# Optimization experiments

Measured on AMD Instinct MI355X. Metric: run time of the kernel, lower is better.

## Reference

```python
import jax, jax.numpy as jnp
import numpy as np
from jax import lax

N_HEAD = 8
C_CLIP = 10.0
NEG_INF = -jnp.inf


def setup_inputs() -> dict:
    key = jax.random.key(0)
    ks = jax.random.split(key, 12)
    B, S, E = 1024, 200, 128
    bound = 1.0 / E
    inp = {
        "encoded_inputs": jax.random.normal(ks[0], (B, S, E), dtype=jnp.float32),
        "demands": jax.random.uniform(ks[1], (B, S), dtype=jnp.float32),
        "capacities": jax.random.uniform(ks[2], (B,), dtype=jnp.float32),
        # learned params
        "vl": jax.random.uniform(ks[3], (1, 1, E), minval=-bound, maxval=bound, dtype=jnp.float32),
        "vf": jax.random.uniform(ks[4], (1, 1, E), minval=-bound, maxval=bound, dtype=jnp.float32),
        "Wq": jax.random.normal(ks[5], (3 * E, E), dtype=jnp.float32) / np.sqrt(3 * E),
        "Wk": jax.random.normal(ks[6], (E, E), dtype=jnp.float32) / np.sqrt(E),
        "Wv": jax.random.normal(ks[7], (E, E), dtype=jnp.float32) / np.sqrt(E),
        "Wo": jax.random.normal(ks[8], (E, E), dtype=jnp.float32) / np.sqrt(E),
        "Wp": jax.random.normal(ks[9], (E, E), dtype=jnp.float32) / np.sqrt(E),  # project_k (no bias)
    }
    return inp


def _decode(encoded_inputs, vl, vf, Wq, Wk, Wv, Wo, Wp):
    B, S, E = encoded_inputs.shape
    H = N_HEAD
    dh = E // H
    scale = jnp.sqrt(jnp.float32(E))
    h_hat = encoded_inputs.mean(axis=1)                       # [B,E] (context mean)
    # keys/values for glimpse MHA and pointer keys are loop-invariant
    k_h = (encoded_inputs @ Wk).reshape(B, S, H, dh).transpose(0, 2, 1, 3)  # [B,H,S,dh]
    v_h = (encoded_inputs @ Wv).reshape(B, S, H, dh).transpose(0, 2, 1, 3)  # [B,H,S,dh]
    k_ptr = encoded_inputs @ Wp                               # [B,S,E]

    mask0 = jnp.zeros((B, S), dtype=bool).at[:, 0].set(True)
    last0 = jnp.broadcast_to(vl[0, 0], (B, E))
    first0 = jnp.broadcast_to(vf[0, 0], (B, E))
    logp0 = jnp.zeros((B,), dtype=jnp.float32)
    rows = jnp.arange(B)

    def step(carry, t):
        mask, last, first, logp = carry
        h_c = jnp.concatenate([h_hat, last, first], axis=-1)  # [B,3E]
        q = (h_c @ Wq).reshape(B, H, dh)
        scores = jnp.einsum('bhd,bhsd->bhs', q, k_h) / jnp.sqrt(jnp.float32(dh))
        scores = jnp.where(mask[:, None, :], NEG_INF, scores)
        attn = jax.nn.softmax(scores, axis=-1)
        ctx = jnp.einsum('bhs,bhsd->bhd', attn, v_h).reshape(B, E) @ Wo   # [B,E]
        u = jnp.tanh(jnp.einsum('be,bse->bs', ctx, k_ptr) / scale) * C_CLIP  # [B,S] raw logits
        u_masked = jnp.where(mask, NEG_INF, u)
        idx = jnp.argmax(u_masked, axis=-1)                   # greedy decoding
        ce = -jnp.take_along_axis(jax.nn.log_softmax(u_masked, axis=-1), idx[:, None], axis=1)[:, 0]
        logp = logp + ce
        last_new = encoded_inputs[rows, idx]                  # [B,E]
        mask_new = mask.at[rows, idx].set(True)
        first_new = jnp.where(t == 0, last_new, first)
        return (mask_new, last_new, first_new, logp), (u, idx)

    (_, _, _, log_probabilities), (raw_u, sols) = lax.scan(
        step, (mask0, last0, first0, logp0), jnp.arange(S - 1))
    raw_logits = raw_u.transpose(1, 0, 2)                     # [B, S-1, S]
    solution = jnp.concatenate([jnp.zeros((B, 1), jnp.int32), sols.T.astype(jnp.int32)], axis=1)
    return raw_logits, log_probabilities, solution


def reference(encoded_inputs, demands, capacities, vl, vf, Wq, Wk, Wv, Wo, Wp):
    # demands/capacities are part of the input tuple but unused by this forward
    return _decode(encoded_inputs, vl, vf, Wq, Wk, Wv, Wo, Wp)
```

## Files before the change

kernel.cpp:

```cpp
#include <hip/hip_runtime.h>
#include <cmath>

constexpr int Bn = 1024, Sn = 200, En = 128, Hn = 8, DHn = 16, Tn = 199;
constexpr long long LOGITS_N = (long long)Bn * Tn * Sn;
constexpr long long LOGP_OFF = LOGITS_N;
constexpr long long SOL_OFF  = LOGP_OFF + Bn;

#define NEG_INF (-__builtin_inff())

__device__ __forceinline__ float dot4(float4 a, float4 b) {
  return a.x * b.x + a.y * b.y + a.z * b.z + a.w * b.w;
}

__global__ __launch_bounds__(128) void hhat_kernel(
    const float* __restrict__ enc, const float* __restrict__ vl, const float* __restrict__ vf,
    const float* __restrict__ Wq, float* __restrict__ qtop, float* __restrict__ qh0)
{
  const int b = blockIdx.x, e = threadIdx.x;
  const float* p = enc + (size_t)b * Sn * En + e;
  float s = 0.f;
  for (int i = 0; i < Sn; ++i) s += p[(size_t)i * En];
  __shared__ float hl[En];
  hl[e] = s * (1.0f / Sn);
  __syncthreads();
  float qt = 0.f, qm = 0.f, qf = 0.f;
#pragma unroll 8
  for (int i = 0; i < En; ++i) {
    qt += hl[i] * Wq[i * En + e];
    qm += vl[i] * Wq[(En + i) * En + e];
    qf += vf[i] * Wq[(2 * En + i) * En + e];
  }
  qtop[(size_t)b * En + e] = qt;
  qh0[(size_t)b * En + e]  = qt + qm + qf;
}

__global__ __launch_bounds__(256) void proj_kernel(
    const float* __restrict__ enc,
    const float* __restrict__ Wk, const float* __restrict__ Wv,
    const float* __restrict__ Wq, const float* __restrict__ Wp,
    float* __restrict__ Kall, float* __restrict__ Vall,
    float* __restrict__ QM, float* __restrict__ KP2)
{
  __shared__ float et[32 * En];
  __shared__ float wl[En * En];
  const int tid = threadIdx.x;
  const size_t r0 = (size_t)blockIdx.x * 32;

  for (int i = tid; i < 32 * En; i += 256) et[i] = enc[r0 * En + i];

  const float* Ws[4] = {Wk, Wv, Wq + (size_t)En * En, Wp};
  float* Os[3] = {Kall, Vall, QM};
  for (int m = 0; m < 4; ++m) {
    __syncthreads();
    const float* W = Ws[m];
    for (int i = tid; i < En * En; i += 256) wl[i] = W[i];
    __syncthreads();
    const int j = tid & 127, half = tid >> 7;
    for (int rr = 0; rr < 16; ++rr) {
      const int r = rr * 2 + half;
      float a0 = 0.f, a1 = 0.f, a2 = 0.f, a3 = 0.f;
#pragma unroll 8
      for (int e = 0; e < En; e += 4) {
        a0 += et[r * En + e    ] * wl[(e    ) * En + j];
        a1 += et[r * En + e + 1] * wl[(e + 1) * En + j];
        a2 += et[r * En + e + 2] * wl[(e + 2) * En + j];
        a3 += et[r * En + e + 3] * wl[(e + 3) * En + j];
      }
      const float a = (a0 + a1) + (a2 + a3);
      const size_t rg = r0 + r;
      if (m < 3) {
        Os[m][rg * En + j] = a;
      } else {
        const int b = (int)(rg / Sn), s = (int)(rg - (size_t)b * Sn);
        KP2[(((size_t)b * 32 + (j >> 2)) * Sn + s) * 4 + (j & 3)] = a;
      }
    }
  }
}

__global__ __launch_bounds__(512, 2) void decode_kernel(
    const float* __restrict__ enc, const float* __restrict__ Wq, const float* __restrict__ Wo,
    const float* __restrict__ Kall, const float* __restrict__ Vall,
    const float* __restrict__ KP2, const float* __restrict__ QM,
    const float* __restrict__ qtop, const float* __restrict__ qh0,
    float* __restrict__ out)
{
  const int b = blockIdx.x, tid = threadIdx.x;
  const int w = tid >> 6, lane = tid & 63;
  const int le = lane & 15, q4 = lane >> 4;

  __shared__ __align__(16) float kp2[32 * Sn * 4];
  __shared__ __align__(16) float qv[En];
  __shared__ __align__(16) float octx[En];
  __shared__ float hqf[En];
  __shared__ float ctxs[En];
  __shared__ float uvals[256];
  __shared__ int   smask[256];
  __shared__ int   idx_s;
  __shared__ float logp_s;

  {
    const float4* src = (const float4*)(KP2 + (size_t)b * (32 * Sn * 4));
    float4* dst = (float4*)kp2;
    for (int i = tid; i < 32 * Sn; i += 512) dst[i] = src[i];
  }
  float Kr[4][16], Vr[4][16];
#pragma unroll
  for (int j = 0; j < 4; ++j) {
    const int s = j * 64 + lane;
    if (s < Sn) {
      const float4* kq = (const float4*)(Kall + ((size_t)b * Sn + s) * En + w * DHn);
      const float4* vq = (const float4*)(Vall + ((size_t)b * Sn + s) * En + w * DHn);
#pragma unroll
      for (int q = 0; q < 4; ++q) {
        const float4 kv = kq[q], vv = vq[q];
        Kr[j][4*q+0] = kv.x; Kr[j][4*q+1] = kv.y; Kr[j][4*q+2] = kv.z; Kr[j][4*q+3] = kv.w;
        Vr[j][4*q+0] = vv.x; Vr[j][4*q+1] = vv.y; Vr[j][4*q+2] = vv.z; Vr[j][4*q+3] = vv.w;
      }
    } else {
#pragma unroll
      for (int d = 0; d < 16; ++d) { Kr[j][d] = 0.f; Vr[j][d] = 0.f; }
    }
  }
  float WoR[32];
  {
    const float* wp = Wo + (size_t)(q4 * 32) * En + (w * DHn + le);
#pragma unroll
    for (int r = 0; r < 32; ++r) WoR[r] = wp[(size_t)r * En];
  }
  if (tid < 256) smask[tid] = (tid == 0) ? 1 : 0;
  if (tid < En)  qv[tid] = qh0[(size_t)b * En + tid];
  if (tid == 0) { logp_s = 0.f; out[SOL_OFF + (size_t)b * Sn] = 0.f; }
  __syncthreads();

  for (int t = 0; t < Tn; ++t) {
    float qs[16];
    {
      const float4* qp = (const float4*)&qv[w * DHn];
#pragma unroll
      for (int q = 0; q < 4; ++q) {
        const float4 v = qp[q];
        qs[4*q+0] = v.x; qs[4*q+1] = v.y; qs[4*q+2] = v.z; qs[4*q+3] = v.w;
      }
    }
    float sc[4];
#pragma unroll
    for (int j = 0; j < 4; ++j) {
      const int s = j * 64 + lane;
      float a = 0.f;
#pragma unroll
      for (int d = 0; d < 16; ++d) a += qs[d] * Kr[j][d];
      sc[j] = (s >= Sn || smask[s]) ? NEG_INF : a * 0.25f;
    }
    float m = fmaxf(fmaxf(sc[0], sc[1]), fmaxf(sc[2], sc[3]));
#pragma unroll
    for (int off = 1; off < 64; off <<= 1) m = fmaxf(m, __shfl_xor(m, off));
    float ev[4]; float sum = 0.f;
#pragma unroll
    for (int j = 0; j < 4; ++j) { ev[j] = expf(sc[j] - m); sum += ev[j]; }
#pragma unroll
    for (int off = 1; off < 64; off <<= 1) sum += __shfl_xor(sum, off);
    const float inv = 1.f / sum;

    float acc[16];
#pragma unroll
    for (int d = 0; d < 16; ++d) acc[d] = 0.f;
#pragma unroll
    for (int j = 0; j < 4; ++j) {
      const float aj = ev[j] * inv;
#pragma unroll
      for (int d = 0; d < 16; ++d) acc[d] += aj * Vr[j][d];
    }
#pragma unroll
    for (int off = 1; off < 64; off <<= 1) {
#pragma unroll
      for (int d = 0; d < 16; ++d) acc[d] += __shfl_xor(acc[d], off);
    }
    if (lane == 0) {
#pragma unroll
      for (int d = 0; d < 16; ++d) ctxs[w * DHn + d] = acc[d];
    }
    __syncthreads();

    {
      float p = 0.f;
      const float* cb = &ctxs[q4 * 32];
#pragma unroll
      for (int r = 0; r < 32; ++r) p += cb[r] * WoR[r];
      p += __shfl_xor(p, 16);
      p += __shfl_xor(p, 32);
      if (lane < 16) octx[w * DHn + le] = p;
    }
    __syncthreads();

    {
      const int sp = tid >> 1, hf = tid & 1;
      float p = 0.f;
      if (sp < Sn) {
        const float4* oc = (const float4*)&octx[hf * 64];
#pragma unroll
        for (int e4 = 0; e4 < 16; ++e4)
          p += dot4(oc[e4], *(const float4*)&kp2[(((hf * 16 + e4) * Sn) + sp) << 2]);
      }
      p += __shfl_xor(p, 1);
      if (!hf) {
        if (sp < Sn) {
          const float uu = tanhf(p * 0.08838834764831845f) * 10.f;
          out[((size_t)b * Tn + t) * Sn + sp] = uu;
          uvals[sp] = smask[sp] ? NEG_INF : uu;
        } else uvals[sp] = NEG_INF;
      }
    }
    __syncthreads();

    if (w == 0) {
      float bv = NEG_INF; int bi = 1 << 30;
#pragma unroll
      for (int k = 0; k < 4; ++k) {
        const int s = lane + 64 * k;
        const float v = uvals[s];
        if (v > bv || (v == bv && s < bi)) { bv = v; bi = s; }
      }
#pragma unroll
      for (int off = 1; off < 64; off <<= 1) {
        const float ovv = __shfl_xor(bv, off); const int oi = __shfl_xor(bi, off);
        if (ovv > bv || (ovv == bv && oi < bi)) { bv = ovv; bi = oi; }
      }
      float sum2 = 0.f;
#pragma unroll
      for (int k = 0; k < 4; ++k) sum2 += expf(uvals[lane + 64 * k] - bv);
#pragma unroll
      for (int off = 1; off < 64; off <<= 1) sum2 += __shfl_xor(sum2, off);
      if (lane == 0) {
        idx_s = bi;
        logp_s += logf(sum2);
        out[SOL_OFF + (size_t)b * Sn + t + 1] = (float)bi;
      }
    }
    __syncthreads();

    const int idx = idx_s;
    if (tid == 0) smask[idx] = 1;

    if (t == 0) {
      if (tid < En) uvals[tid] = enc[((size_t)b * Sn + idx) * En + tid];
      __syncthreads();
      {
        float p = 0.f;
        const float* er  = &uvals[q4 * 32];
        const float* wqb = Wq + (size_t)(2 * En + q4 * 32) * En + (w * DHn + le);
#pragma unroll
        for (int r = 0; r < 32; ++r) p += er[r] * wqb[(size_t)r * En];
        p += __shfl_xor(p, 16);
        p += __shfl_xor(p, 32);
        if (lane < 16) hqf[w * DHn + le] = qtop[(size_t)b * En + (w * DHn + le)] + p;
      }
      __syncthreads();
    }

    if (t + 1 < Tn) {
      if (tid < En) qv[tid] = hqf[tid] + QM[((size_t)b * Sn + idx) * En + tid];
    }
    __syncthreads();
  }
  if (tid == 0) out[LOGP_OFF + b] = logp_s;
}

extern "C" void kernel_launch(void* const* d_in, const int* in_sizes, int n_in,
                              void* d_out, int out_size, void* d_ws, size_t ws_size,
                              hipStream_t stream)
{
  const float* enc = (const float*)d_in[0];
  const float* vl  = (const float*)d_in[3];
  const float* vf  = (const float*)d_in[4];
  const float* Wq  = (const float*)d_in[5];
  const float* Wk  = (const float*)d_in[6];
  const float* Wv  = (const float*)d_in[7];
  const float* Wo  = (const float*)d_in[8];
  const float* Wp  = (const float*)d_in[9];
  float* out = (float*)d_out;

  float* ws   = (float*)d_ws;
  const size_t BSE = (size_t)Bn * Sn * En;
  float* Kall = ws;
  float* Vall = Kall + BSE;
  float* QM   = Vall + BSE;
  float* KP2  = QM   + BSE;
  float* qtop = KP2  + BSE;
  float* qh0  = qtop + (size_t)Bn * En;

  hipLaunchKernelGGL(hhat_kernel, dim3(Bn), dim3(En), 0, stream, enc, vl, vf, Wq, qtop, qh0);
  hipLaunchKernelGGL(proj_kernel, dim3((Bn * Sn) / 32), dim3(256), 0, stream,
                     enc, Wk, Wv, Wq, Wp, Kall, Vall, QM, KP2);
  hipLaunchKernelGGL(decode_kernel, dim3(Bn), dim3(512), 0, stream,
                     enc, Wq, Wo, Kall, Vall, KP2, QM, qtop, qh0, out);
}
```

Baseline: 6.255 ms.

## Restructure decode loop: register-resident pointer keys, shared QM, fewer barriers

The decode kernel now keeps the pointer-key projection in registers, split per head-wave, instead of in shared memory. It stages the QM table in LDS so the next-step query is formed in place. The mask moves into per-lane register bits, argmax runs redundantly in every wave to drop a barrier, the ctx reduction uses a transpose-style butterfly, and tanh/exp switch to fast intrinsics. The projection kernel is re-tiled to register-block 16 rows and to write K/V in the head-interleaved layout. The cost is higher register pressure (three 64-float arrays per thread), a launch-bounds change that drops the 2-blocks hint, and about 100KB of LDS per block.

```diff
diff --git a/kernel.cpp b/kernel.cpp
--- a/kernel.cpp
+++ b/kernel.cpp
@@ -7,10 +7,6 @@
 constexpr long long SOL_OFF  = LOGP_OFF + Bn;
 
 #define NEG_INF (-__builtin_inff())
-
-__device__ __forceinline__ float dot4(float4 a, float4 b) {
-  return a.x * b.x + a.y * b.y + a.z * b.z + a.w * b.w;
-}
 
 __global__ __launch_bounds__(128) void hhat_kernel(
     const float* __restrict__ enc, const float* __restrict__ vl, const float* __restrict__ vf,
@@ -38,7 +34,7 @@
     const float* __restrict__ enc,
     const float* __restrict__ Wk, const float* __restrict__ Wv,
     const float* __restrict__ Wq, const float* __restrict__ Wp,
-    float* __restrict__ Kall, float* __restrict__ Vall,
+    float* __restrict__ K2, float* __restrict__ V2,
     float* __restrict__ QM, float* __restrict__ KP2)
 {
   __shared__ float et[32 * En];
@@ -49,38 +45,43 @@
   for (int i = tid; i < 32 * En; i += 256) et[i] = enc[r0 * En + i];
 
   const float* Ws[4] = {Wk, Wv, Wq + (size_t)En * En, Wp};
-  float* Os[3] = {Kall, Vall, QM};
+  const int j = tid & 127, half = tid >> 7;
   for (int m = 0; m < 4; ++m) {
     __syncthreads();
     const float* W = Ws[m];
     for (int i = tid; i < En * En; i += 256) wl[i] = W[i];
     __syncthreads();
-    const int j = tid & 127, half = tid >> 7;
-    for (int rr = 0; rr < 16; ++rr) {
-      const int r = rr * 2 + half;
-      float a0 = 0.f, a1 = 0.f, a2 = 0.f, a3 = 0.f;
-#pragma unroll 8
-      for (int e = 0; e < En; e += 4) {
-        a0 += et[r * En + e    ] * wl[(e    ) * En + j];
-        a1 += et[r * En + e + 1] * wl[(e + 1) * En + j];
-        a2 += et[r * En + e + 2] * wl[(e + 2) * En + j];
-        a3 += et[r * En + e + 3] * wl[(e + 3) * En + j];
-      }
-      const float a = (a0 + a1) + (a2 + a3);
-      const size_t rg = r0 + r;
-      if (m < 3) {
-        Os[m][rg * En + j] = a;
+    float a[16];
+#pragma unroll
+    for (int r = 0; r < 16; ++r) a[r] = 0.f;
+    for (int e = 0; e < En; e += 4) {
+      const float w0 = wl[(e    ) * En + j];
+      const float w1 = wl[(e + 1) * En + j];
+      const float w2 = wl[(e + 2) * En + j];
+      const float w3 = wl[(e + 3) * En + j];
+#pragma unroll
+      for (int r = 0; r < 16; ++r) {
+        const float4 e4 = *(const float4*)&et[(r * 2 + half) * En + e];
+        a[r] += e4.x * w0 + e4.y * w1 + e4.z * w2 + e4.w * w3;
+      }
+    }
+#pragma unroll
+    for (int r = 0; r < 16; ++r) {
+      const size_t rg = r0 + r * 2 + half;
+      const int b = (int)(rg / Sn), s = (int)(rg - (size_t)b * Sn);
+      if (m == 2) {
+        QM[rg * En + j] = a[r];
       } else {
-        const int b = (int)(rg / Sn), s = (int)(rg - (size_t)b * Sn);
-        KP2[(((size_t)b * 32 + (j >> 2)) * Sn + s) * 4 + (j & 3)] = a;
+        float* o = (m == 0) ? K2 : (m == 1) ? V2 : KP2;
+        o[(((size_t)b * 32 + (j >> 2)) * Sn + s) * 4 + (j & 3)] = a[r];
       }
     }
   }
 }
 
-__global__ __launch_bounds__(512, 2) void decode_kernel(
+__global__ __launch_bounds__(512) void decode_kernel(
     const float* __restrict__ enc, const float* __restrict__ Wq, const float* __restrict__ Wo,
-    const float* __restrict__ Kall, const float* __restrict__ Vall,
+    const float* __restrict__ K2, const float* __restrict__ V2,
     const float* __restrict__ KP2, const float* __restrict__ QM,
     const float* __restrict__ qtop, const float* __restrict__ qh0,
     float* __restrict__ out)
@@ -88,38 +89,42 @@
   const int b = blockIdx.x, tid = threadIdx.x;
   const int w = tid >> 6, lane = tid & 63;
   const int le = lane & 15, q4 = lane >> 4;
-
-  __shared__ __align__(16) float kp2[32 * Sn * 4];
-  __shared__ __align__(16) float qv[En];
-  __shared__ __align__(16) float octx[En];
+  const int dm = ((le & 1) << 3) | ((le & 2) << 1) | ((le & 4) >> 1) | ((le & 8) >> 3);
+
+  __shared__ __align__(16) float qmL[Sn * En];
+  __shared__ __align__(16) float ctxp[4 * 36];
+  __shared__ float part[8 * 257];
+  __shared__ float uvals[256];
   __shared__ float hqf[En];
-  __shared__ float ctxs[En];
-  __shared__ float uvals[256];
-  __shared__ int   smask[256];
-  __shared__ int   idx_s;
-  __shared__ float logp_s;
+  __shared__ float ebuf[En];
 
   {
-    const float4* src = (const float4*)(KP2 + (size_t)b * (32 * Sn * 4));
-    float4* dst = (float4*)kp2;
-    for (int i = tid; i < 32 * Sn; i += 512) dst[i] = src[i];
-  }
-  float Kr[4][16], Vr[4][16];
+    const float4* src = (const float4*)(QM + (size_t)b * Sn * En);
+    float4* dst = (float4*)qmL;
+    for (int i = tid; i < Sn * En / 4; i += 512) dst[i] = src[i];
+  }
+  if (tid < En) hqf[tid] = qh0[(size_t)b * En + tid];
+  if (tid >= 200 && tid < 256) uvals[tid] = NEG_INF;
+  if (tid == 0) out[SOL_OFF + (size_t)b * Sn] = 0.f;
+
+  float Kr[4][16], Vr[4][16], KPr[4][16];
 #pragma unroll
   for (int j = 0; j < 4; ++j) {
     const int s = j * 64 + lane;
     if (s < Sn) {
-      const float4* kq = (const float4*)(Kall + ((size_t)b * Sn + s) * En + w * DHn);
-      const float4* vq = (const float4*)(Vall + ((size_t)b * Sn + s) * En + w * DHn);
 #pragma unroll
       for (int q = 0; q < 4; ++q) {
-        const float4 kv = kq[q], vv = vq[q];
+        const size_t base = (((size_t)b * 32 + w * 4 + q) * Sn + s) * 4;
+        const float4 kv = *(const float4*)(K2 + base);
+        const float4 vv = *(const float4*)(V2 + base);
+        const float4 pv = *(const float4*)(KP2 + base);
         Kr[j][4*q+0] = kv.x; Kr[j][4*q+1] = kv.y; Kr[j][4*q+2] = kv.z; Kr[j][4*q+3] = kv.w;
         Vr[j][4*q+0] = vv.x; Vr[j][4*q+1] = vv.y; Vr[j][4*q+2] = vv.z; Vr[j][4*q+3] = vv.w;
+        KPr[j][4*q+0] = pv.x; KPr[j][4*q+1] = pv.y; KPr[j][4*q+2] = pv.z; KPr[j][4*q+3] = pv.w;
       }
     } else {
 #pragma unroll
-      for (int d = 0; d < 16; ++d) { Kr[j][d] = 0.f; Vr[j][d] = 0.f; }
+      for (int d = 0; d < 16; ++d) { Kr[j][d] = 0.f; Vr[j][d] = 0.f; KPr[j][d] = 0.f; }
     }
   }
   float WoR[32];
@@ -128,142 +133,144 @@
 #pragma unroll
     for (int r = 0; r < 32; ++r) WoR[r] = wp[(size_t)r * En];
   }
-  if (tid < 256) smask[tid] = (tid == 0) ? 1 : 0;
-  if (tid < En)  qv[tid] = qh0[(size_t)b * En + tid];
-  if (tid == 0) { logp_s = 0.f; out[SOL_OFF + (size_t)b * Sn] = 0.f; }
+
+  unsigned mreg = (lane == 0 ? 1u : 0u) | (lane >= 8 ? 8u : 0u);
+  float logp = 0.f;
+  int idx = 0;
   __syncthreads();
 
   for (int t = 0; t < Tn; ++t) {
-    float qs[16];
-    {
-      const float4* qp = (const float4*)&qv[w * DHn];
-#pragma unroll
-      for (int q = 0; q < 4; ++q) {
-        const float4 v = qp[q];
-        qs[4*q+0] = v.x; qs[4*q+1] = v.y; qs[4*q+2] = v.z; qs[4*q+3] = v.w;
-      }
-    }
-    float sc[4];
-#pragma unroll
-    for (int j = 0; j < 4; ++j) {
-      const int s = j * 64 + lane;
-      float a = 0.f;
-#pragma unroll
-      for (int d = 0; d < 16; ++d) a += qs[d] * Kr[j][d];
-      sc[j] = (s >= Sn || smask[s]) ? NEG_INF : a * 0.25f;
-    }
-    float m = fmaxf(fmaxf(sc[0], sc[1]), fmaxf(sc[2], sc[3]));
+    float sc4[4] = {0.f, 0.f, 0.f, 0.f};
+#pragma unroll
+    for (int c = 0; c < 4; ++c) {
+      const float4 hv = *(const float4*)&hqf[w * DHn + 4 * c];
+      float q0 = hv.x, q1 = hv.y, q2 = hv.z, q3 = hv.w;
+      if (t) {
+        const float4 qm4 = *(const float4*)&qmL[idx * En + w * DHn + 4 * c];
+        q0 += qm4.x; q1 += qm4.y; q2 += qm4.z; q3 += qm4.w;
+      }
+#pragma unroll
+      for (int jj = 0; jj < 4; ++jj)
+        sc4[jj] += q0 * Kr[jj][4*c] + q1 * Kr[jj][4*c+1] + q2 * Kr[jj][4*c+2] + q3 * Kr[jj][4*c+3];
+    }
+    float m = NEG_INF;
+#pragma unroll
+    for (int jj = 0; jj < 4; ++jj) {
+      sc4[jj] = ((mreg >> jj) & 1u) ? NEG_INF : sc4[jj] * 0.25f;
+      m = fmaxf(m, sc4[jj]);
+    }
 #pragma unroll
     for (int off = 1; off < 64; off <<= 1) m = fmaxf(m, __shfl_xor(m, off));
     float ev[4]; float sum = 0.f;
 #pragma unroll
-    for (int j = 0; j < 4; ++j) { ev[j] = expf(sc[j] - m); sum += ev[j]; }
+    for (int jj = 0; jj < 4; ++jj) { ev[jj] = __expf(sc4[jj] - m); sum += ev[jj]; }
 #pragma unroll
     for (int off = 1; off < 64; off <<= 1) sum += __shfl_xor(sum, off);
     const float inv = 1.f / sum;
 
-    float acc[16];
-#pragma unroll
-    for (int d = 0; d < 16; ++d) acc[d] = 0.f;
-#pragma unroll
-    for (int j = 0; j < 4; ++j) {
-      const float aj = ev[j] * inv;
-#pragma unroll
-      for (int d = 0; d < 16; ++d) acc[d] += aj * Vr[j][d];
+    float red[16];
+#pragma unroll
+    for (int d = 0; d < 16; ++d) red[d] = 0.f;
+#pragma unroll
+    for (int jj = 0; jj < 4; ++jj) {
+      const float aj = ev[jj] * inv;
+#pragma unroll
+      for (int d = 0; d < 16; ++d) red[d] += aj * Vr[jj][d];
+    }
+#pragma unroll
+    for (int k = 0; k < 4; ++k) {
+      const int off = 1 << k, h = 8 >> k;
+#pragma unroll
+      for (int i = 0; i < 8; ++i) {
+        if (i < h) {
+          const bool up = (lane & off) != 0;
+          const float send = up ? red[i] : red[i + h];
+          const float keep = up ? red[i + h] : red[i];
+          red[i] = keep + __shfl_xor(send, off);
+        }
+      }
+    }
+    red[0] += __shfl_xor(red[0], 16);
+    red[0] += __shfl_xor(red[0], 32);
+    if (lane < 16) {
+      const int d = w * DHn + dm;
+      ctxp[(d >> 5) * 36 + (d & 31)] = red[0];
+    }
+    __syncthreads();
+
+    float p = 0.f;
+#pragma unroll
+    for (int c = 0; c < 8; ++c) {
+      const float4 cv = *(const float4*)&ctxp[q4 * 36 + 4 * c];
+      p += cv.x * WoR[4*c] + cv.y * WoR[4*c+1] + cv.z * WoR[4*c+2] + cv.w * WoR[4*c+3];
+    }
+    p += __shfl_xor(p, 16);
+    p += __shfl_xor(p, 32);
+
+    float up[4] = {0.f, 0.f, 0.f, 0.f};
+#pragma unroll
+    for (int d = 0; d < 16; ++d) {
+      const float od = __shfl(p, d);
+#pragma unroll
+      for (int jj = 0; jj < 4; ++jj) up[jj] += od * KPr[jj][d];
+    }
+#pragma unroll
+    for (int jj = 0; jj < 4; ++jj) part[w * 257 + jj * 64 + lane] = up[jj];
+    __syncthreads();
+
+    if (tid < Sn) {
+      float u = 0.f;
+#pragma unroll
+      for (int ww = 0; ww < 8; ++ww) u += part[ww * 257 + tid];
+      const float e2 = __expf(u * (2.f * 0.08838834764831845f));
+      const float uu = 10.f * (1.f - 2.f / (e2 + 1.f));
+      out[((size_t)b * Tn + t) * Sn + tid] = uu;
+      uvals[tid] = uu;
+    }
+    __syncthreads();
+
+    float bv = NEG_INF; int bi = 1 << 30;
+    float vk[4];
+#pragma unroll
+    for (int k = 0; k < 4; ++k) {
+      const int s = k * 64 + lane;
+      const float v = ((mreg >> k) & 1u) ? NEG_INF : uvals[s];
+      vk[k] = v;
+      if (v > bv || (v == bv && s < bi)) { bv = v; bi = s; }
     }
 #pragma unroll
     for (int off = 1; off < 64; off <<= 1) {
-#pragma unroll
-      for (int d = 0; d < 16; ++d) acc[d] += __shfl_xor(acc[d], off);
-    }
-    if (lane == 0) {
-#pragma unroll
-      for (int d = 0; d < 16; ++d) ctxs[w * DHn + d] = acc[d];
-    }
-    __syncthreads();
-
-    {
-      float p = 0.f;
-      const float* cb = &ctxs[q4 * 32];
-#pragma unroll
-      for (int r = 0; r < 32; ++r) p += cb[r] * WoR[r];
-      p += __shfl_xor(p, 16);
-      p += __shfl_xor(p, 32);
-      if (lane < 16) octx[w * DHn + le] = p;
-    }
-    __syncthreads();
-
-    {
-      const int sp = tid >> 1, hf = tid & 1;
-      float p = 0.f;
-      if (sp < Sn) {
-        const float4* oc = (const float4*)&octx[hf * 64];
-#pragma unroll
-        for (int e4 = 0; e4 < 16; ++e4)
-          p += dot4(oc[e4], *(const float4*)&kp2[(((hf * 16 + e4) * Sn) + sp) << 2]);
-      }
-      p += __shfl_xor(p, 1);
-      if (!hf) {
-        if (sp < Sn) {
-          const float uu = tanhf(p * 0.08838834764831845f) * 10.f;
-          out[((size_t)b * Tn + t) * Sn + sp] = uu;
-          uvals[sp] = smask[sp] ? NEG_INF : uu;
-        } else uvals[sp] = NEG_INF;
-      }
-    }
-    __syncthreads();
-
+      const float ov = __shfl_xor(bv, off); const int oi = __shfl_xor(bi, off);
+      if (ov > bv || (ov == bv && oi < bi)) { bv = ov; bi = oi; }
+    }
+    idx = bi;
+    if ((idx & 63) == lane) mreg |= 1u << (idx >> 6);
     if (w == 0) {
-      float bv = NEG_INF; int bi = 1 << 30;
-#pragma unroll
-      for (int k = 0; k < 4; ++k) {
-        const int s = lane + 64 * k;
-        const float v = uvals[s];
-        if (v > bv || (v == bv && s < bi)) { bv = v; bi = s; }
-      }
-#pragma unroll
-      for (int off = 1; off < 64; off <<= 1) {
-        const float ovv = __shfl_xor(bv, off); const int oi = __shfl_xor(bi, off);
-        if (ovv > bv || (ovv == bv && oi < bi)) { bv = ovv; bi = oi; }
-      }
-      float sum2 = 0.f;
-#pragma unroll
-      for (int k = 0; k < 4; ++k) sum2 += expf(uvals[lane + 64 * k] - bv);
-#pragma unroll
-      for (int off = 1; off < 64; off <<= 1) sum2 += __shfl_xor(sum2, off);
+      float s2 = 0.f;
+#pragma unroll
+      for (int k = 0; k < 4; ++k) s2 += __expf(vk[k] - bv);
+#pragma unroll
+      for (int off = 1; off < 64; off <<= 1) s2 += __shfl_xor(s2, off);
       if (lane == 0) {
-        idx_s = bi;
-        logp_s += logf(sum2);
+        logp += __logf(s2);
         out[SOL_OFF + (size_t)b * Sn + t + 1] = (float)bi;
       }
     }
-    __syncthreads();
-
-    const int idx = idx_s;
-    if (tid == 0) smask[idx] = 1;
 
     if (t == 0) {
-      if (tid < En) uvals[tid] = enc[((size_t)b * Sn + idx) * En + tid];
+      if (tid < En) ebuf[tid] = enc[((size_t)b * Sn + idx) * En + tid];
       __syncthreads();
-      {
-        float p = 0.f;
-        const float* er  = &uvals[q4 * 32];
-        const float* wqb = Wq + (size_t)(2 * En + q4 * 32) * En + (w * DHn + le);
-#pragma unroll
-        for (int r = 0; r < 32; ++r) p += er[r] * wqb[(size_t)r * En];
-        p += __shfl_xor(p, 16);
-        p += __shfl_xor(p, 32);
-        if (lane < 16) hqf[w * DHn + le] = qtop[(size_t)b * En + (w * DHn + le)] + p;
-      }
+      float pb = 0.f;
+#pragma unroll 8
+      for (int r = 0; r < 32; ++r)
+        pb += ebuf[q4 * 32 + r] * Wq[(size_t)(2 * En + q4 * 32 + r) * En + (w * DHn + le)];
+      pb += __shfl_xor(pb, 16);
+      pb += __shfl_xor(pb, 32);
+      if (lane < 16) hqf[w * DHn + le] = qtop[(size_t)b * En + w * DHn + le] + pb;
       __syncthreads();
     }
-
-    if (t + 1 < Tn) {
-      if (tid < En) qv[tid] = hqf[tid] + QM[((size_t)b * Sn + idx) * En + tid];
-    }
-    __syncthreads();
-  }
-  if (tid == 0) out[LOGP_OFF + b] = logp_s;
+  }
+  if (tid == 0) out[LOGP_OFF + b] = logp;
 }
 
 extern "C" void kernel_launch(void* const* d_in, const int* in_sizes, int n_in,
@@ -282,16 +289,16 @@
 
   float* ws   = (float*)d_ws;
   const size_t BSE = (size_t)Bn * Sn * En;
-  float* Kall = ws;
-  float* Vall = Kall + BSE;
-  float* QM   = Vall + BSE;
-  float* KP2  = QM   + BSE;
-  float* qtop = KP2  + BSE;
+  float* K2   = ws;
+  float* V2   = K2  + BSE;
+  float* QM   = V2  + BSE;
+  float* KP2  = QM  + BSE;
+  float* qtop = KP2 + BSE;
   float* qh0  = qtop + (size_t)Bn * En;
 
   hipLaunchKernelGGL(hhat_kernel, dim3(Bn), dim3(En), 0, stream, enc, vl, vf, Wq, qtop, qh0);
   hipLaunchKernelGGL(proj_kernel, dim3((Bn * Sn) / 32), dim3(256), 0, stream,
-                     enc, Wk, Wv, Wq, Wp, Kall, Vall, QM, KP2);
+                     enc, Wk, Wv, Wq, Wp, K2, V2, QM, KP2);
   hipLaunchKernelGGL(decode_kernel, dim3(Bn), dim3(512), 0, stream,
-                     enc, Wq, Wo, Kall, Vall, KP2, QM, qtop, qh0, out);
+                     enc, Wq, Wo, K2, V2, KP2, QM, qtop, qh0, out);
 }
```

After: 13.63 ms. 2.18x slower.
